# Performance work log

Hardware: AMD Instinct MI355X
Metric: run time of the kernel (lower is better)

Reference implementation:

```python
import jax, jax.numpy as jnp
import numpy as np

WIN_LENGTH = 5  # window size (five-in-a-row)


def setup_inputs() -> dict:
    key = jax.random.key(0)
    point_input = jax.random.normal(key, (128, 16, 128, 128), dtype=jnp.float32)
    return {"point_input": point_input}


def reference(point_input) -> jnp.ndarray:
    # Directional box sums of length WIN_LENGTH centered at each board point,
    # zero padding outside the board (equivalent to conv2d with the diag-embedded
    # all-ones kernel and padding = WIN_LENGTH // 2).
    L = WIN_LENGTH
    p = L // 2
    N, C, H, W = point_input.shape
    xp = jnp.pad(point_input, ((0, 0), (0, 0), (p, p), (p, p)))
    # horizontal: sum along W window
    hor = sum(xp[:, :, p:p + H, d:d + W] for d in range(L))
    # vertical: sum along H window
    ver = sum(xp[:, :, d:d + H, p:p + W] for d in range(L))
    # main diagonal (dH == dW)
    diag = sum(xp[:, :, d:d + H, d:d + W] for d in range(L))
    # anti-diagonal (dH == -dW)
    adiag = sum(xp[:, :, d:d + H, (L - 1 - d):(L - 1 - d) + W] for d in range(L))
    # (N, 4*C, H, W)
    return jnp.concatenate([hor, ver, diag, adiag], axis=1)
```

## Files before the change

kernel.cpp:

```cpp
#include <hip/hip_runtime.h>


constexpr int N = 128, C = 16, H = 128, W = 128;
constexpr int TH = 32, TW = 128;
constexpr int HALO = 2;
constexpr int LH = TH + 2 * HALO;
constexpr int LW = TW + 2 * HALO;

__global__ __launch_bounds__(256, 8)
void Point2DirSum_kernel(const float* __restrict__ in, float* __restrict__ out) {
    __shared__ __align__(16) float tile[LH * LW];
    const int tid = threadIdx.x;
    constexpr int TILES_PER_IMG = H / TH;
    const int img = blockIdx.x / TILES_PER_IMG;
    const int t   = blockIdx.x % TILES_PER_IMG;
    const int h0  = t * TH;
    const float* __restrict__ inp = in + (size_t)img * H * W;

    for (int idx = tid; idx < LH * LW; idx += 256) {
        const int r  = idx / LW;
        const int cc = idx - r * LW;
        const int h  = h0 + r - HALO;
        const int w  = cc - HALO;
        float v = 0.0f;
        if ((unsigned)h < (unsigned)H && (unsigned)w < (unsigned)W)
            v = inp[h * W + w];
        tile[idx] = v;
    }
    __syncthreads();

    const int n = img / C;
    const int c = img - n * C;
    float* __restrict__ outp = out + (((size_t)n * 4 * C + c) * (size_t)H) * W;
    const size_t plane = (size_t)C * H * W;

    constexpr int GROUPS = TH * TW / 4;
    for (int g = tid; g < GROUPS; g += 256) {
        const int rl = g >> 5;
        const int w4 = (g & 31) * 4;

        float ho[4], ve[4], di[4], ad[4];
        #pragma unroll
        for (int j = 0; j < 4; ++j) { ve[j] = 0.f; di[j] = 0.f; ad[j] = 0.f; }

        #pragma unroll
        for (int d = 0; d < 5; ++d) {
            const float4 a = *(const float4*)&tile[(rl + d) * LW + w4];
            const float4 b = *(const float4*)&tile[(rl + d) * LW + w4 + 4];
            float e[8];
            e[0] = a.x; e[1] = a.y; e[2] = a.z; e[3] = a.w;
            e[4] = b.x; e[5] = b.y; e[6] = b.z; e[7] = b.w;
            #pragma unroll
            for (int j = 0; j < 4; ++j) {
                ve[j] += e[j + 2];
                di[j] += e[j + d];
                ad[j] += e[j + 4 - d];
            }
            if (d == 2) {
                #pragma unroll
                for (int j = 0; j < 4; ++j)
                    ho[j] = e[j] + e[j + 1] + e[j + 2] + e[j + 3] + e[j + 4];
            }
        }

        const int h = h0 + rl;
        const size_t o = (size_t)h * W + w4;
        *(float4*)&outp[o]             = make_float4(ho[0], ho[1], ho[2], ho[3]);
        *(float4*)&outp[o + plane]     = make_float4(ve[0], ve[1], ve[2], ve[3]);
        *(float4*)&outp[o + 2 * plane] = make_float4(di[0], di[1], di[2], di[3]);
        *(float4*)&outp[o + 3 * plane] = make_float4(ad[0], ad[1], ad[2], ad[3]);
    }
}

extern "C" void kernel_launch(void* const* d_in, const int* in_sizes, int n_in,
                              void* d_out, int out_size, void* d_ws, size_t ws_size,
                              hipStream_t stream) {
    const float* in = (const float*)d_in[0];
    float* out = (float*)d_out;
    const int grid = N * C * (H / TH);
    Point2DirSum_kernel<<<grid, 256, 0, stream>>>(in, out);
}
```

Before: 619.8 us.

## Replace shared-memory tile with register sliding window and nontemporal stores

Drops the LDS tile and barrier. Each thread now loads its rows straight from global memory (float4 plus float2 halos) and keeps a 4-row vertical register window, so each loaded row feeds several output rows. Output writes use nontemporal stores to avoid polluting the cache. Launch bounds are relaxed to 4 waves to allow more registers. Neighbouring threads' halo loads overlap and are served by cache, and lower occupancy may reduce latency hiding.

```diff
diff --git a/kernel.cpp b/kernel.cpp
--- a/kernel.cpp
+++ b/kernel.cpp
@@ -1,74 +1,84 @@
 #include <hip/hip_runtime.h>
 
 
+typedef float f32x4 __attribute__((ext_vector_type(4)));
+
 constexpr int N = 128, C = 16, H = 128, W = 128;
-constexpr int TH = 32, TW = 128;
-constexpr int HALO = 2;
-constexpr int LH = TH + 2 * HALO;
-constexpr int LW = TW + 2 * HALO;
+constexpr int TH = 32;
+constexpr int VB = 4;
 
-__global__ __launch_bounds__(256, 8)
+__global__ __launch_bounds__(256, 4)
 void Point2DirSum_kernel(const float* __restrict__ in, float* __restrict__ out) {
-    __shared__ __align__(16) float tile[LH * LW];
     const int tid = threadIdx.x;
     constexpr int TILES_PER_IMG = H / TH;
     const int img = blockIdx.x / TILES_PER_IMG;
     const int t   = blockIdx.x % TILES_PER_IMG;
     const int h0  = t * TH;
-    const float* __restrict__ inp = in + (size_t)img * H * W;
 
-    for (int idx = tid; idx < LH * LW; idx += 256) {
-        const int r  = idx / LW;
-        const int cc = idx - r * LW;
-        const int h  = h0 + r - HALO;
-        const int w  = cc - HALO;
-        float v = 0.0f;
-        if ((unsigned)h < (unsigned)H && (unsigned)w < (unsigned)W)
-            v = inp[h * W + w];
-        tile[idx] = v;
+    const int w4 = (tid & 31) * 4;
+    const int hb = h0 + (tid >> 5) * VB;
+
+    const float* __restrict__ base =
+        in + (size_t)img * H * W + (size_t)(hb - 2) * W + (w4 - 2);
+
+    const bool c_lo = (w4 != 0);
+    const bool c_hi = (w4 != W - 4);
+
+    float ve[VB][4], di[VB][4], ad[VB][4], ho[VB][4];
+    #pragma unroll
+    for (int i = 0; i < VB; ++i)
+        #pragma unroll
+        for (int j = 0; j < 4; ++j) { ve[i][j] = 0.f; di[i][j] = 0.f; ad[i][j] = 0.f; }
+
+    #pragma unroll
+    for (int r = 0; r < VB + 4; ++r) {
+        const int gr = hb - 2 + r;
+        const bool rok = (unsigned)gr < (unsigned)H;
+        float e[8];
+        #pragma unroll
+        for (int k = 0; k < 8; ++k) e[k] = 0.f;
+        if (rok) {
+            const float* rp = base + r * W;
+            const float4 m = *(const float4*)(rp + 2);
+            e[2] = m.x; e[3] = m.y; e[4] = m.z; e[5] = m.w;
+            if (c_lo) { const float2 lo = *(const float2*)(rp);     e[0] = lo.x; e[1] = lo.y; }
+            if (c_hi) { const float2 hi = *(const float2*)(rp + 6); e[6] = hi.x; e[7] = hi.y; }
+        }
+        #pragma unroll
+        for (int i = 0; i < VB; ++i) {
+            const int d = r - i;
+            if (d >= 0 && d < 5) {
+                #pragma unroll
+                for (int j = 0; j < 4; ++j) {
+                    ve[i][j] += e[j + 2];
+                    di[i][j] += e[j + d];
+                    ad[i][j] += e[j + 4 - d];
+                }
+                if (d == 2) {
+                    #pragma unroll
+                    for (int j = 0; j < 4; ++j)
+                        ho[i][j] = e[j] + e[j + 1] + e[j + 2] + e[j + 3] + e[j + 4];
+                }
+            }
+        }
     }
-    __syncthreads();
 
     const int n = img / C;
     const int c = img - n * C;
     float* __restrict__ outp = out + (((size_t)n * 4 * C + c) * (size_t)H) * W;
     const size_t plane = (size_t)C * H * W;
 
-    constexpr int GROUPS = TH * TW / 4;
-    for (int g = tid; g < GROUPS; g += 256) {
-        const int rl = g >> 5;
-        const int w4 = (g & 31) * 4;
-
-        float ho[4], ve[4], di[4], ad[4];
-        #pragma unroll
-        for (int j = 0; j < 4; ++j) { ve[j] = 0.f; di[j] = 0.f; ad[j] = 0.f; }
-
-        #pragma unroll
-        for (int d = 0; d < 5; ++d) {
-            const float4 a = *(const float4*)&tile[(rl + d) * LW + w4];
-            const float4 b = *(const float4*)&tile[(rl + d) * LW + w4 + 4];
-            float e[8];
-            e[0] = a.x; e[1] = a.y; e[2] = a.z; e[3] = a.w;
-            e[4] = b.x; e[5] = b.y; e[6] = b.z; e[7] = b.w;
-            #pragma unroll
-            for (int j = 0; j < 4; ++j) {
-                ve[j] += e[j + 2];
-                di[j] += e[j + d];
-                ad[j] += e[j + 4 - d];
-            }
-            if (d == 2) {
-                #pragma unroll
-                for (int j = 0; j < 4; ++j)
-                    ho[j] = e[j] + e[j + 1] + e[j + 2] + e[j + 3] + e[j + 4];
-            }
-        }
-
-        const int h = h0 + rl;
-        const size_t o = (size_t)h * W + w4;
-        *(float4*)&outp[o]             = make_float4(ho[0], ho[1], ho[2], ho[3]);
-        *(float4*)&outp[o + plane]     = make_float4(ve[0], ve[1], ve[2], ve[3]);
-        *(float4*)&outp[o + 2 * plane] = make_float4(di[0], di[1], di[2], di[3]);
-        *(float4*)&outp[o + 3 * plane] = make_float4(ad[0], ad[1], ad[2], ad[3]);
+    #pragma unroll
+    for (int i = 0; i < VB; ++i) {
+        const size_t o = (size_t)(hb + i) * W + w4;
+        f32x4 vho = { ho[i][0], ho[i][1], ho[i][2], ho[i][3] };
+        f32x4 vve = { ve[i][0], ve[i][1], ve[i][2], ve[i][3] };
+        f32x4 vdi = { di[i][0], di[i][1], di[i][2], di[i][3] };
+        f32x4 vad = { ad[i][0], ad[i][1], ad[i][2], ad[i][3] };
+        __builtin_nontemporal_store(vho, (f32x4*)&outp[o]);
+        __builtin_nontemporal_store(vve, (f32x4*)&outp[o + plane]);
+        __builtin_nontemporal_store(vdi, (f32x4*)&outp[o + 2 * plane]);
+        __builtin_nontemporal_store(vad, (f32x4*)&outp[o + 3 * plane]);
     }
 }
 
```

Result: no change. 608.0 us (-1.9%).
